# Kernel tuning notes

Hardware: AMD Instinct MI355X
Metric: run time of the kernel (lower is better)

## Reference

```python
import jax, jax.numpy as jnp
import numpy as np

B, N, KNN_K, T_FRAC = 8, 4096, 32, 0.5
C_IN, C_OUT = 4, 64


def _knn_group(q, db, kk):
    """q: [Nq,3] queries, db: [Nd,3] database. Returns feats [Nq,kk,4], nn [Nq,kk,3]."""
    d2 = (jnp.sum(q * q, axis=-1, keepdims=True)
          + jnp.sum(db * db, axis=-1)[None, :]
          - 2.0 * (q @ db.T))                      # [Nq,Nd] squared dists
    _, idx = jax.lax.top_k(-d2, kk)                 # ascending distance, like pytorch3d knn_points
    nn = db[idx]                                    # [Nq,kk,3]
    resi = nn - q[:, None, :]                       # [Nq,kk,3]
    sq = jnp.sum(resi * resi, axis=-1, keepdims=True)
    dist = jnp.where(sq > 0, jnp.sqrt(jnp.where(sq > 0, sq, 1.0)), 0.0)  # safe norm (exact fwd)
    feats = jnp.concatenate([resi, dist], axis=-1)  # [Nq,kk,4]
    return feats, nn


def _forward(points1, points2, pc, Wq, Wk, Wv, bq, bk, bv, ridx1, ridx2, k, t):
    k2 = int(k * t)
    k1 = k - k2
    p1 = jnp.swapaxes(points1, 1, 2)  # [B,N,3]
    p2 = jnp.swapaxes(points2, 1, 2)
    p3 = jnp.swapaxes(pc, 1, 2)

    def per_batch(a, b, c, i1, i2):
        newp = jnp.concatenate([a[i1], b[i2]], axis=0)     # [N,3] fused candidate set
        f1, g1 = _knn_group(newp, a, k1)
        f2, g2 = _knn_group(newp, b, k2)
        f3, g3 = _knn_group(newp, c, k)
        feats = jnp.concatenate([f1, f2, f3], axis=1)      # [N,2k,4]
        grouped = jnp.concatenate([g1, g2, g3], axis=1)    # [N,2k,3]
        return feats, grouped

    feats, grouped = jax.vmap(per_batch)(p1, p2, p3, ridx1, ridx2)  # [B,N,2k,4], [B,N,2k,3]

    # SelfAttention over the neighbor axis (per point group)
    q = feats @ Wq + bq          # [B,N,2k,C_OUT]
    kf = feats @ Wk + bk
    v = feats @ Wv + bv
    scale = 1.0 / np.sqrt(C_OUT).astype(np.float32)
    attn = jax.nn.softmax(jnp.einsum('bnkc,bnjc->bnkj', q, kf) * scale, axis=-1)
    y = jnp.einsum('bnkj,bnjc->bnkc', attn, v)             # [B,N,2k,C_OUT]

    score = jnp.max(y, axis=-1)                            # max over channels -> [B,N,2k]
    w = jax.nn.softmax(score, axis=-1)                     # weights over 2k neighbors
    fused = jnp.einsum('bnk,bnkd->bdn', w, grouped)        # [B,3,N]
    return fused


def setup_inputs() -> dict:
    key = jax.random.key(0)
    ks = jax.random.split(key, 8)
    points1 = jax.random.normal(ks[0], (B, 3, N), dtype=jnp.float32)
    points2 = jax.random.normal(ks[1], (B, 3, N), dtype=jnp.float32)
    pc = jax.random.normal(ks[2], (B, 3, N), dtype=jnp.float32)
    N2 = int(N * T_FRAC)
    N1 = N - N2
    perm = lambda kk: jax.random.permutation(kk, N)
    ridx1 = jax.vmap(perm)(jax.random.split(ks[3], B))[:, :N1].astype(jnp.int32)
    ridx2 = jax.vmap(perm)(jax.random.split(ks[4], B))[:, :N2].astype(jnp.int32)
    s = 1.0 / np.sqrt(C_IN)
    Wq = jax.random.normal(ks[5], (C_IN, C_OUT), dtype=jnp.float32) * s
    Wk = jax.random.normal(ks[6], (C_IN, C_OUT), dtype=jnp.float32) * s
    Wv = jax.random.normal(ks[7], (C_IN, C_OUT), dtype=jnp.float32) * s
    z = jnp.zeros((C_OUT,), dtype=jnp.float32)
    return {"points1": points1, "points2": points2, "pc": pc,
            "Wq": Wq, "Wk": Wk, "Wv": Wv, "bq": z, "bk": z, "bv": z,
            "ridx1": ridx1, "ridx2": ridx2, "k": KNN_K, "t": T_FRAC}


def reference(points1, points2, pc, Wq, Wk, Wv, bq, bk, bv, ridx1, ridx2, k, t):
    return _forward(points1, points2, pc, Wq, Wk, Wv, bq, bk, bv, ridx1, ridx2, k, t)
```

## Files before the change

### kernel.cpp

```cpp
#include <hip/hip_runtime.h>
#include <hip/hip_bf16.h>
#include <math.h>

#define NB   8
#define NPT  4096
#define NQ1  2048
#define NQ2  2048
#define KTOT 64
#define TILE 512
#define NTHR 128
#define QPB  64
#define TBUF 16
#define MPAD 33

#define PRM_OFF (4u << 20)

__global__ void pf2_setup(const float* __restrict__ Wq, const float* __restrict__ Wk,
                          const float* __restrict__ bq, const float* __restrict__ bk,
                          float* __restrict__ prm) {
    int t = threadIdx.x;
    const float sc = 0.125f;
    if (t < 16) {
        int p = t >> 2, q = t & 3;
        float a = 0.f;
        for (int c = 0; c < 64; ++c) a += Wq[p * 64 + c] * Wk[q * 64 + c];
        prm[t] = a * sc;
    } else if (t < 20) {
        int p = t - 16; float a = 0.f;
        for (int c = 0; c < 64; ++c) a += Wq[p * 64 + c] * bk[c];
        prm[t] = a * sc;
    } else if (t < 24) {
        int q = t - 20; float a = 0.f;
        for (int c = 0; c < 64; ++c) a += Wk[q * 64 + c] * bq[c];
        prm[t] = a * sc;
    } else if (t == 24) {
        float a = 0.f;
        for (int c = 0; c < 64; ++c) a += bq[c] * bk[c];
        prm[t] = a * sc;
    }
}

template <int K>
__device__ __forceinline__ void insert_med3(float (&dl)[K], int (&il)[K], float d, int id) {
    float pd = -INFINITY; int pi = 0;
    bool cp = false;
#pragma unroll
    for (int j = 0; j < K; ++j) {
        float oj = dl[j]; int ij = il[j];
        bool cj = d < oj;
        dl[j] = __builtin_amdgcn_fmed3f(d, pd, oj);
        il[j] = cp ? pi : (cj ? id : ij);
        pd = oj; pi = ij; cp = cj;
    }
}

template <int K>
__device__ void knn_half(const float* __restrict__ dbp,
                         float qx, float qy, float qz, int tid,
                         float4* __restrict__ tileLds,
                         unsigned short* __restrict__ bufLds,
                         float* __restrict__ mD,
                         unsigned short* __restrict__ mI,
                         unsigned short* __restrict__ outIdx) {
    const int q = tid & (QPB - 1), h = tid >> 6;
    float dl[K]; int il[K];
#pragma unroll
    for (int j = 0; j < K; ++j) { dl[j] = INFINITY; il[j] = 0; }
    float thresh = INFINITY;
    int cnt = 0;
    float4* tp = tileLds + h * TILE;

    for (int st = 0; st < 2048 / TILE; ++st) {
        int base = h * 2048 + st * TILE;
        __syncthreads();
        for (int r = 0; r < TILE / QPB; ++r) {
            int j = q + r * QPB;
            float x = dbp[base + j];
            float y = dbp[NPT + base + j];
            float z = dbp[2 * NPT + base + j];
            tp[j] = make_float4(-2.f * x, -2.f * y, -2.f * z,
                                fmaf(x, x, fmaf(y, y, z * z)));
        }
        __syncthreads();

        for (int c0 = 0; c0 < TILE; c0 += 8) {
            float sv[8];
#pragma unroll
            for (int u = 0; u < 8; ++u) {
                float4 p = tp[c0 + u];
                sv[u] = fmaf(p.x, qx, fmaf(p.y, qy, fmaf(p.z, qz, p.w)));
            }
#pragma unroll
            for (int u = 0; u < 8; ++u) {
                if (sv[u] < thresh) {
                    bufLds[cnt * NTHR + tid] = (unsigned short)(c0 + u);
                    ++cnt;
                }
            }
            if (__any(cnt > TBUF - 8)) {
                for (int u = 0; u < TBUF; ++u) {
                    if (!__any(u < cnt)) break;
                    if (u < cnt) {
                        int j = bufLds[u * NTHR + tid];
                        float4 p = tp[j];
                        float s = fmaf(p.x, qx, fmaf(p.y, qy, fmaf(p.z, qz, p.w)));
                        if (s < dl[K - 1]) insert_med3<K>(dl, il, s, base + j);
                    }
                }
                cnt = 0;
                thresh = dl[K - 1];
            }
        }
        for (int u = 0; u < TBUF; ++u) {
            if (!__any(u < cnt)) break;
            if (u < cnt) {
                int j = bufLds[u * NTHR + tid];
                float4 p = tp[j];
                float s = fmaf(p.x, qx, fmaf(p.y, qy, fmaf(p.z, qz, p.w)));
                if (s < dl[K - 1]) insert_med3<K>(dl, il, s, base + j);
            }
        }
        cnt = 0;
        thresh = dl[K - 1];
    }

    __syncthreads();
    if (h == 1) {
#pragma unroll
        for (int j = 0; j < K; ++j) {
            mD[q * MPAD + j] = dl[j];
            mI[q * MPAD + j] = (unsigned short)il[j];
        }
    }
    __syncthreads();
    if (h == 0) {
#pragma unroll
        for (int j = 0; j < K; ++j) {
            float d = mD[q * MPAD + j];
            int id = (int)mI[q * MPAD + j];
            if (d < dl[K - 1]) insert_med3<K>(dl, il, d, id);
        }
        unsigned* o32 = (unsigned*)outIdx;
#pragma unroll
        for (int u = 0; u < K / 2; ++u)
            o32[u] = (unsigned)(unsigned short)il[2 * u] |
                     ((unsigned)(unsigned short)il[2 * u + 1] << 16);
    }
}

__global__ __launch_bounds__(NTHR) void pf2_knn(const float* __restrict__ p1,
                                                const float* __restrict__ p2,
                                                const float* __restrict__ pc,
                                                const int* __restrict__ ridx1,
                                                const int* __restrict__ ridx2,
                                                unsigned short* __restrict__ wsIdx) {
    __shared__ float4 tileLds[2 * TILE];
    __shared__ unsigned short bufLds[TBUF * NTHR];
    float* mD = (float*)tileLds;
    unsigned short* mI = (unsigned short*)(mD + QPB * MPAD);

    int bid = blockIdx.x;
    int chunk = bid & 63;
    int db = (bid >> 6) % 3;
    int b = bid / 192;
    int tid = threadIdx.x;
    int i = chunk * QPB + (tid & (QPB - 1));

    int j0; const float* srcp;
    if (i < NQ1) { j0 = ridx1[b * NQ1 + i]; srcp = p1; }
    else         { j0 = ridx2[b * NQ2 + (i - NQ1)]; srcp = p2; }
    const float* sb = srcp + (size_t)b * 3 * NPT;
    float qx = sb[j0], qy = sb[NPT + j0], qz = sb[2 * NPT + j0];

    const float* dbp = (db == 0 ? p1 : db == 1 ? p2 : pc) + (size_t)b * 3 * NPT;
    unsigned short* out = wsIdx + (size_t)(b * NPT + i) * KTOT +
                          (db == 0 ? 0 : db == 1 ? 16 : 32);
    if (db < 2) knn_half<16>(dbp, qx, qy, qz, tid, tileLds, bufLds, mD, mI, out);
    else        knn_half<32>(dbp, qx, qy, qz, tid, tileLds, bufLds, mD, mI, out);
}

__global__ __launch_bounds__(256) void pf2_attn(const float* __restrict__ p1,
                                                const float* __restrict__ p2,
                                                const float* __restrict__ pc,
                                                const int* __restrict__ ridx1,
                                                const int* __restrict__ ridx2,
                                                const float* __restrict__ Wv,
                                                const float* __restrict__ bv,
                                                const float* __restrict__ prm,
                                                const unsigned short* __restrict__ wsIdx,
                                                float* __restrict__ out) {
    __shared__ float4 wvt[64];
    __shared__ float  bvs[64];
    __shared__ float  prms[25];
    __shared__ float4 gl[4][64];
    __shared__ float4 fl[4][64];
    __shared__ float  sl[4][64];

    int tid = threadIdx.x;
    if (tid < 64) {
        wvt[tid] = make_float4(Wv[tid], Wv[64 + tid], Wv[128 + tid], Wv[192 + tid]);
        bvs[tid] = bv[tid];
    } else if (tid < 89) {
        prms[tid - 64] = prm[tid - 64];
    }
    __syncthreads();

    int wv = tid >> 6, lane = tid & 63;
    int g = blockIdx.x * 4 + wv;
    int b = g >> 12;
    int i = g & 4095;

    int j0; const float* srcp;
    if (i < NQ1) { j0 = ridx1[b * NQ1 + i]; srcp = p1; }
    else         { j0 = ridx2[b * NQ2 + (i - NQ1)]; srcp = p2; }
    const float* sb = srcp + (size_t)b * 3 * NPT;
    float qx = sb[j0], qy = sb[NPT + j0], qz = sb[2 * NPT + j0];

    int nidx = (int)wsIdx[(size_t)(b * NPT + i) * KTOT + lane];
    const float* dbp = (lane < 16 ? p1 : lane < 32 ? p2 : pc) + (size_t)b * 3 * NPT;
    float nx = dbp[nidx], ny = dbp[NPT + nidx], nz = dbp[2 * NPT + nidx];
    float fx = nx - qx, fy = ny - qy, fz = nz - qz;
    float sq = fx * fx + fy * fy + fz * fz;
    float fw = sq > 0.f ? sqrtf(sq) : 0.f;

    float gx = prms[0]  * fx + prms[1]  * fy + prms[2]  * fz + prms[3]  * fw;
    float gy = prms[4]  * fx + prms[5]  * fy + prms[6]  * fz + prms[7]  * fw;
    float gz = prms[8]  * fx + prms[9]  * fy + prms[10] * fz + prms[11] * fw;
    float gw = prms[12] * fx + prms[13] * fy + prms[14] * fz + prms[15] * fw;
    float sj = prms[20] * fx + prms[21] * fy + prms[22] * fz + prms[23] * fw;

    gl[wv][lane] = make_float4(gx, gy, gz, gw);
    fl[wv][lane] = make_float4(fx, fy, fz, fw);
    sl[wv][lane] = sj;
    __syncthreads();

    float m = -INFINITY;
    for (int j = 0; j < 64; ++j) {
        float4 gj = gl[wv][j];
        float l = fx * gj.x + fy * gj.y + fz * gj.z + fw * gj.w + sl[wv][j];
        m = fmaxf(m, l);
    }
    float S = 0.f, H0 = 0.f, H1 = 0.f, H2 = 0.f, H3 = 0.f;
    for (int j = 0; j < 64; ++j) {
        float4 gj = gl[wv][j];
        float4 fj = fl[wv][j];
        float l = fx * gj.x + fy * gj.y + fz * gj.z + fw * gj.w + sl[wv][j];
        float e = __expf(l - m);
        S += e;
        H0 += e * fj.x; H1 += e * fj.y; H2 += e * fj.z; H3 += e * fj.w;
    }
    float rS = 1.f / S;

    float smax = -INFINITY;
    for (int ch = 0; ch < 64; ++ch) {
        float4 wc = wvt[ch];
        float t = H0 * wc.x + H1 * wc.y + H2 * wc.z + H3 * wc.w;
        float yv = fmaf(t, rS, bvs[ch]);
        smax = fmaxf(smax, yv);
    }

    float M = smax;
    for (int off = 32; off; off >>= 1) M = fmaxf(M, __shfl_xor(M, off));
    float e = __expf(smax - M);
    float E = e;
    for (int off = 32; off; off >>= 1) E += __shfl_xor(E, off);
    float w = e / E;
    float px = w * nx, py = w * ny, pz = w * nz;
    for (int off = 32; off; off >>= 1) {
        px += __shfl_xor(px, off);
        py += __shfl_xor(py, off);
        pz += __shfl_xor(pz, off);
    }
    if (lane == 0) {
        float* ob = out + (size_t)b * 3 * NPT + i;
        ob[0] = px; ob[NPT] = py; ob[2 * NPT] = pz;
    }
}

extern "C" void kernel_launch(void* const* d_in, const int* in_sizes, int n_in,
                              void* d_out, int out_size, void* d_ws, size_t ws_size,
                              hipStream_t stream) {
    const float* p1 = (const float*)d_in[0];
    const float* p2 = (const float*)d_in[1];
    const float* pc = (const float*)d_in[2];
    const float* Wq = (const float*)d_in[3];
    const float* Wk = (const float*)d_in[4];
    const float* Wv = (const float*)d_in[5];
    const float* bq = (const float*)d_in[6];
    const float* bk = (const float*)d_in[7];
    const float* bv = (const float*)d_in[8];
    const int* ridx1 = (const int*)d_in[9];
    const int* ridx2 = (const int*)d_in[10];
    float* out = (float*)d_out;

    unsigned short* wsIdx = (unsigned short*)d_ws;
    float* prm = (float*)((char*)d_ws + PRM_OFF);

    pf2_setup<<<1, 32, 0, stream>>>(Wq, Wk, bq, bk, prm);
    pf2_knn<<<NB * 3 * (NPT / QPB), NTHR, 0, stream>>>(p1, p2, pc, ridx1, ridx2, wsIdx);
    pf2_attn<<<NB * NPT / 4, 256, 0, stream>>>(p1, p2, pc, ridx1, ridx2, Wv, bv, prm, wsIdx, out);
}
```

Measured before the change: 469.0 us.

## Widen kNN blocks to 256 threads, enlarge candidate buffer, reorder block schedule

The kNN kernel now runs 256 threads per block with 128 queries, still split into two database halves. The per-thread candidate buffer grows from 16 to 48 entries, so full flushes into the sorted list happen less often. Early flushes at fixed points in the first tile tighten the threshold sooner. Blocks are reordered so the heavier K=32 database runs first, and the merge scratch uses a transposed, conflict-free layout. The cost is more LDS per block, which may lower occupancy.

Result: slower. 518.7 us (+10.6%).

```diff
diff --git a/kernel.cpp b/kernel.cpp
--- a/kernel.cpp
+++ b/kernel.cpp
@@ -8,10 +8,9 @@
 #define NQ2  2048
 #define KTOT 64
 #define TILE 512
-#define NTHR 128
-#define QPB  64
-#define TBUF 16
-#define MPAD 33
+#define NTHR 256
+#define QPB  128
+#define CAP  48
 
 #define PRM_OFF (4u << 20)
 
@@ -59,19 +58,32 @@
                          float qx, float qy, float qz, int tid,
                          float4* __restrict__ tileLds,
                          unsigned short* __restrict__ bufLds,
-                         float* __restrict__ mD,
-                         unsigned short* __restrict__ mI,
                          unsigned short* __restrict__ outIdx) {
-    const int q = tid & (QPB - 1), h = tid >> 6;
+    const int q = tid & (QPB - 1), h = tid >> 7;
     float dl[K]; int il[K];
 #pragma unroll
     for (int j = 0; j < K; ++j) { dl[j] = INFINITY; il[j] = 0; }
     float thresh = INFINITY;
     int cnt = 0;
     float4* tp = tileLds + h * TILE;
+    int base = 0;
+
+    auto flush = [&]() {
+        for (int u = 0; u < CAP; ++u) {
+            if (!__any(u < cnt)) break;
+            if (u < cnt) {
+                int j = bufLds[u * NTHR + tid];
+                float4 p = tp[j];
+                float s = fmaf(p.x, qx, fmaf(p.y, qy, fmaf(p.z, qz, p.w)));
+                if (s < dl[K - 1]) insert_med3<K>(dl, il, s, base + j);
+            }
+        }
+        cnt = 0;
+        thresh = dl[K - 1];
+    };
 
     for (int st = 0; st < 2048 / TILE; ++st) {
-        int base = h * 2048 + st * TILE;
+        base = h * 2048 + st * TILE;
         __syncthreads();
         for (int r = 0; r < TILE / QPB; ++r) {
             int j = q + r * QPB;
@@ -97,47 +109,28 @@
                     ++cnt;
                 }
             }
-            if (__any(cnt > TBUF - 8)) {
-                for (int u = 0; u < TBUF; ++u) {
-                    if (!__any(u < cnt)) break;
-                    if (u < cnt) {
-                        int j = bufLds[u * NTHR + tid];
-                        float4 p = tp[j];
-                        float s = fmaf(p.x, qx, fmaf(p.y, qy, fmaf(p.z, qz, p.w)));
-                        if (s < dl[K - 1]) insert_med3<K>(dl, il, s, base + j);
-                    }
-                }
-                cnt = 0;
-                thresh = dl[K - 1];
-            }
-        }
-        for (int u = 0; u < TBUF; ++u) {
-            if (!__any(u < cnt)) break;
-            if (u < cnt) {
-                int j = bufLds[u * NTHR + tid];
-                float4 p = tp[j];
-                float s = fmaf(p.x, qx, fmaf(p.y, qy, fmaf(p.z, qz, p.w)));
-                if (s < dl[K - 1]) insert_med3<K>(dl, il, s, base + j);
-            }
-        }
-        cnt = 0;
-        thresh = dl[K - 1];
-    }
-
+            if (__any(cnt >= CAP - 8)) flush();
+            else if (st == 0 && (c0 == 56 || c0 == 120 || c0 == 248)) flush();
+        }
+        flush();
+    }
+
+    float* mD = (float*)tileLds;
+    unsigned short* mI = bufLds;
     __syncthreads();
     if (h == 1) {
 #pragma unroll
         for (int j = 0; j < K; ++j) {
-            mD[q * MPAD + j] = dl[j];
-            mI[q * MPAD + j] = (unsigned short)il[j];
+            mD[j * QPB + q] = dl[j];
+            mI[j * QPB + q] = (unsigned short)il[j];
         }
     }
     __syncthreads();
     if (h == 0) {
 #pragma unroll
         for (int j = 0; j < K; ++j) {
-            float d = mD[q * MPAD + j];
-            int id = (int)mI[q * MPAD + j];
+            float d = mD[j * QPB + q];
+            int id = (int)mI[j * QPB + q];
             if (d < dl[K - 1]) insert_med3<K>(dl, il, d, id);
         }
         unsigned* o32 = (unsigned*)outIdx;
@@ -155,14 +148,14 @@
                                                 const int* __restrict__ ridx2,
                                                 unsigned short* __restrict__ wsIdx) {
     __shared__ float4 tileLds[2 * TILE];
-    __shared__ unsigned short bufLds[TBUF * NTHR];
-    float* mD = (float*)tileLds;
-    unsigned short* mI = (unsigned short*)(mD + QPB * MPAD);
+    __shared__ unsigned short bufLds[CAP * NTHR];
 
     int bid = blockIdx.x;
-    int chunk = bid & 63;
-    int db = (bid >> 6) % 3;
-    int b = bid / 192;
+    int dbslot = bid >> 8;
+    int db = (dbslot == 0) ? 2 : dbslot - 1;
+    int rem = bid & 255;
+    int b = rem >> 5;
+    int chunk = rem & 31;
     int tid = threadIdx.x;
     int i = chunk * QPB + (tid & (QPB - 1));
 
@@ -175,8 +168,8 @@
     const float* dbp = (db == 0 ? p1 : db == 1 ? p2 : pc) + (size_t)b * 3 * NPT;
     unsigned short* out = wsIdx + (size_t)(b * NPT + i) * KTOT +
                           (db == 0 ? 0 : db == 1 ? 16 : 32);
-    if (db < 2) knn_half<16>(dbp, qx, qy, qz, tid, tileLds, bufLds, mD, mI, out);
-    else        knn_half<32>(dbp, qx, qy, qz, tid, tileLds, bufLds, mD, mI, out);
+    if (db < 2) knn_half<16>(dbp, qx, qy, qz, tid, tileLds, bufLds, out);
+    else        knn_half<32>(dbp, qx, qy, qz, tid, tileLds, bufLds, out);
 }
 
 __global__ __launch_bounds__(256) void pf2_attn(const float* __restrict__ p1,
```
